# Kernel tuning notes

Hardware: AMD Instinct MI355X
Metric: run time of the kernel (lower is better)

## Reference

```python
import jax, jax.numpy as jnp
import numpy as np

B, NP, DL, DA, H, NB = 8, 81920, 16, 4, 128, 3
DT_TOTAL = DL + DA  # 20
NSTEPS = 4
DT = 0.1


def setup_inputs() -> dict:
    key = jax.random.key(0)
    k1, k2, k3, k4 = jax.random.split(key, 4)
    inputs = jax.random.normal(k1, (B, NP, DT_TOTAL), dtype=jnp.float32)
    neighbours = jax.random.randint(k2, (NP, NB), 0, NP, dtype=jnp.int64)
    fan_in = NB * DT_TOTAL  # 60
    W1 = jax.random.normal(k3, (fan_in, H), dtype=jnp.float32) / np.sqrt(fan_in)
    b1 = jnp.zeros((H,), dtype=jnp.float32)
    W2 = jax.random.normal(k4, (H, DL), dtype=jnp.float32) / np.sqrt(H)
    b2 = jnp.zeros((DL,), dtype=jnp.float32)
    return {"inputs": inputs, "neighbours": neighbours, "W1": W1, "b1": b1, "W2": W2, "b2": b2}


def reference(inputs, neighbours, W1, b1, W2, b2):
    """nsteps of forward Euler: Y[..., :DL] += dt * Phi(gather(Y, neighbours))."""
    Y = inputs
    for _ in range(NSTEPS):
        # neighbour gather: (B, NP, NB, DT_TOTAL)
        Z = Y[:, neighbours, :]
        # shared interaction MLP on flattened neighbourhood features
        Zf = Z.reshape(B, NP, NB * DT_TOTAL)
        h = jnp.tanh(jnp.einsum('bpf,fh->bph', Zf, W1) + b1)
        fZ = jnp.einsum('bph,hd->bpd', h, W2) + b2  # (B, NP, DL)
        # pad with zeros over ancillary dims == update only latent slice
        Y = Y.at[..., :DL].add(DT * fZ)
    return Y
```

## Files before the change

### kernel.cpp

```cpp
#include <hip/hip_runtime.h>

#define B_DIM   8
#define NPTS    81920
#define DTOT    20
#define DT_STEP 0.1f

#define BLOCK 64
#define GRID  5120
#define ITERS 8
#define NFRAG 21
#define FIMG_BYTES 32768
#define TANH_SCALE 2.885390082f

#define MDL_ROW 32
#define MDA_ROW 8

typedef __attribute__((ext_vector_type(8))) short    short8;
typedef __attribute__((ext_vector_type(4))) float    f32x4;
typedef __attribute__((ext_vector_type(2))) unsigned u32x2;
typedef __attribute__((ext_vector_type(4))) unsigned u32x4;
typedef __attribute__((ext_vector_type(2))) short    short2v;

__device__ __forceinline__ unsigned short f2bf(float f) {
    unsigned u = __builtin_bit_cast(unsigned, f);
    u += 0x7FFFu + ((u >> 16) & 1u);
    return (unsigned short)(u >> 16);
}
#if __has_builtin(__builtin_amdgcn_cvt_pk_bf16_f32)
__device__ __forceinline__ unsigned pack2(float a, float b) {
    short2v p = __builtin_amdgcn_cvt_pk_bf16_f32(a, b);
    return __builtin_bit_cast(unsigned, p);
}
#else
__device__ __forceinline__ unsigned pack2(float a, float b) {
    return (unsigned)f2bf(a) | ((unsigned)f2bf(b) << 16);
}
#endif
__device__ __forceinline__ f32x4 unpack4(u32x2 m) {
    f32x4 o;
    o.x = __builtin_bit_cast(float, m.x << 16);
    o.y = __builtin_bit_cast(float, m.x & 0xffff0000u);
    o.z = __builtin_bit_cast(float, m.y << 16);
    o.w = __builtin_bit_cast(float, m.y & 0xffff0000u);
    return o;
}
__device__ __forceinline__ float tanh_folded(float a) {
    float e = __builtin_amdgcn_exp2f(a);
    float r = __builtin_amdgcn_rcpf(1.0f + e);
    return 1.0f - 2.0f * r;
}

__device__ __forceinline__ int feat_of(int ks, int q, int j) {
    if (ks == 0) {
        if (q == 0) return j;
        if (q == 1) return 8 + j;
        if (q == 2) return 20 + j;
        return (j < 4) ? 16 + j : 36 + (j - 4);
    }
    if (q == 0) return 28 + j;
    if (q == 1) return 40 + j;
    if (q == 2) return 48 + j;
    if (j < 4) return 56 + j;
    return (j == 4) ? 60 : 61;
}

__device__ __forceinline__ int hid_of(int ks, int q, int j) {
    return (2 * ks + (j >> 2)) * 16 + q * 4 + (j & 3);
}

__global__ __launch_bounds__(256) void build_mirror(
    const f32x4* __restrict__ in, char* __restrict__ m0dl,
    char* __restrict__ mda, f32x4* __restrict__ outF, int n4,
    const float* __restrict__ W1, const float* __restrict__ b1,
    const float* __restrict__ W2, const float* __restrict__ b2,
    char* __restrict__ img)
{
    const int i = blockIdx.x * 256 + threadIdx.x;
    if (i < n4) {
        f32x4 v = in[i];
        u32x2 o; o.x = pack2(v.x, v.y); o.y = pack2(v.z, v.w);
        const int r = i / 5, c = i % 5;
        if (c < 4) {
            *(u32x2*)(m0dl + (size_t)r * MDL_ROW + c * 8) = o;
        } else {
            *(u32x2*)(mda + (size_t)r * MDA_ROW) = o;
            outF[i] = v;
        }
    }
    if (blockIdx.x == 0) {
        const int t = threadIdx.x, lane = t & 63, g = t >> 6;
        const int l15 = lane & 15, q = lane >> 4;
        for (int f = g; f < NFRAG; f += 4) {
            char* dst = img + (f * 64 + lane) * 16;
            if (f < 16) {
                const int nt = f >> 1, ks = f & 1, m = nt * 16 + l15;
                unsigned short v[8];
                #pragma unroll
                for (int j = 0; j < 8; j++) {
                    const int ft = feat_of(ks, q, j);
                    float x = (ft < 60) ? TANH_SCALE * W1[ft * 128 + m]
                                        : (ft == 60 ? TANH_SCALE * b1[m] : 0.0f);
                    v[j] = f2bf(x);
                }
                *(u32x4*)dst = *(const u32x4*)v;
            } else if (f < 20) {
                const int ks = f - 16;
                unsigned short v[8];
                #pragma unroll
                for (int j = 0; j < 8; j++) {
                    const int H = hid_of(ks, q, j);
                    v[j] = f2bf(DT_STEP * W2[H * 16 + l15]);
                }
                *(u32x4*)dst = *(const u32x4*)v;
            } else {
                f32x4 a = { DT_STEP * b2[q * 4 + 0], DT_STEP * b2[q * 4 + 1],
                            DT_STEP * b2[q * 4 + 2], DT_STEP * b2[q * 4 + 3] };
                *(f32x4*)dst = a;
            }
        }
    }
}

__device__ __forceinline__ void gather3(
    const char* __restrict__ MdlB, const char* __restrict__ MdaB,
    int nx0, int nx1, int nx2,
    int offA, int offB, bool selA, bool selB, bool q3,
    u32x4& A, u32x4& Bv, u32x2& C)
{
    const int rA = selA ? nx1 : nx0;
    const int rB = selB ? nx2 : nx1;
    const char* aA = q3 ? (MdaB + (size_t)nx0 * MDA_ROW)
                        : (MdlB + (size_t)rA * MDL_ROW + offA);
    const char* aB = q3 ? (MdaB + (size_t)nx1 * MDA_ROW)
                        : (MdlB + (size_t)rB * MDL_ROW + offB);
    A  = *(const u32x4*)aA;
    Bv = *(const u32x4*)aB;
    u32x2 c = { 0u, 0u };
    if (q3) c = *(const u32x2*)(MdaB + (size_t)nx2 * MDA_ROW);
    C = c;
}

__global__ __launch_bounds__(BLOCK) void neural_step(
    float* __restrict__ Yout,
    const char* __restrict__ Mdl_in, char* __restrict__ Mdl_out,
    const char* __restrict__ Mda,
    const int* __restrict__ nbr, const char* __restrict__ img,
    const int last)
{
    const int t = threadIdx.x, lane = t & 63;
    const int l15 = lane & 15, q = lane >> 4;
    const bool q3 = (q == 3);
    const bool selA = (q == 2);
    const bool selB = (q == 1) || (q == 2);
    const int offA = (q == 1) ? 16 : 0;
    const int offB = (q == 0) || (q == 2) ? 16 : 0;

    const int bk = blockIdx.x;
    const int bB = bk & 7;
    const int p0 = (bk >> 3) * (ITERS * 16) + l15;
    const size_t rowBase = (size_t)bB * NPTS;
    const char* MdlB = Mdl_in  + (size_t)bB * NPTS * MDL_ROW;
    char*       MdoB = Mdl_out + (size_t)bB * NPTS * MDL_ROW;
    const char* MdaB = Mda     + (size_t)bB * NPTS * MDA_ROW;

    int nx0, nx1, nx2, ny0 = 0, ny1 = 0, ny2 = 0;
    u32x4 gA, gB, nA = {0,0,0,0}, nB = {0,0,0,0};
    u32x2 gC, nC = {0,0};
    u32x2 ownC, ownN = {0u, 0u};
    {
        const int* np = nbr + (size_t)p0 * 3;
        nx0 = np[0]; nx1 = np[1]; nx2 = np[2];
        gather3(MdlB, MdaB, nx0, nx1, nx2, offA, offB, selA, selB, q3,
                gA, gB, gC);
        ownC = *(const u32x2*)(MdlB + (size_t)p0 * MDL_ROW + q * 8);
        const int* np1 = nbr + (size_t)(p0 + 16) * 3;
        nx0 = np1[0]; nx1 = np1[1]; nx2 = np1[2];
    }

    const short8* frg = (const short8*)img;
    short8 B1f[8][2];
    #pragma unroll
    for (int nt = 0; nt < 8; nt++)
        #pragma unroll
        for (int ks = 0; ks < 2; ks++)
            B1f[nt][ks] = frg[(nt * 2 + ks) * 64 + lane];
    short8 W2f[4];
    #pragma unroll
    for (int ks = 0; ks < 4; ks++)
        W2f[ks] = frg[(16 + ks) * 64 + lane];
    const f32x4 acc2init = ((const f32x4*)img)[20 * 64 + lane];

    #pragma unroll
    for (int it = 0; it < ITERS; it++) {
        if (it + 1 < ITERS) {
            ownN = *(const u32x2*)(MdlB + (size_t)(p0 + (it + 1) * 16) * MDL_ROW
                                   + q * 8);
            gather3(MdlB, MdaB, nx0, nx1, nx2, offA, offB, selA, selB, q3,
                    nA, nB, nC);
        }
        if (it + 2 < ITERS) {
            const int* np = nbr + (size_t)(p0 + (it + 2) * 16) * 3;
            ny0 = np[0]; ny1 = np[1]; ny2 = np[2];
        }

        u32x4 u0 = { gA.x, gA.y, q3 ? gB.x : gA.z, q3 ? gB.y : gA.w };
        u32x4 u1 = { q3 ? gC.x : gB.x, q3 ? gC.y : gB.y,
                     q3 ? 0x00003F80u : gB.z, q3 ? 0u : gB.w };
        short8 zb0 = __builtin_bit_cast(short8, u0);
        short8 zb1 = __builtin_bit_cast(short8, u1);

        unsigned hx[8], hy[8];
        #pragma unroll
        for (int nt = 0; nt < 8; nt++) {
            f32x4 acc = { 0.f, 0.f, 0.f, 0.f };
            acc = __builtin_amdgcn_mfma_f32_16x16x32_bf16(B1f[nt][0], zb0, acc, 0, 0, 0);
            acc = __builtin_amdgcn_mfma_f32_16x16x32_bf16(B1f[nt][1], zb1, acc, 0, 0, 0);
            hx[nt] = pack2(tanh_folded(acc[0]), tanh_folded(acc[1]));
            hy[nt] = pack2(tanh_folded(acc[2]), tanh_folded(acc[3]));
        }

        f32x4 acc2 = acc2init;
        #pragma unroll
        for (int ks = 0; ks < 4; ks++) {
            u32x4 hu = { hx[2 * ks], hy[2 * ks], hx[2 * ks + 1], hy[2 * ks + 1] };
            acc2 = __builtin_amdgcn_mfma_f32_16x16x32_bf16(
                W2f[ks], __builtin_bit_cast(short8, hu), acc2, 0, 0, 0);
        }

        f32x4 o = unpack4(ownC);
        o.x += acc2[0]; o.y += acc2[1]; o.z += acc2[2]; o.w += acc2[3];
        if (!last) {
            char* mrow = MdoB + (size_t)(p0 + it * 16) * MDL_ROW;
            u32x2 mw; mw.x = pack2(o.x, o.y); mw.y = pack2(o.z, o.w);
            *(u32x2*)(mrow + q * 8) = mw;
        } else {
            const size_t row = rowBase + (size_t)(p0 + it * 16);
            __builtin_nontemporal_store(o, (f32x4*)(Yout + row * DTOT) + q);
        }

        ownC = ownN;
        gA = nA; gB = nB; gC = nC;
        nx0 = ny0; nx1 = ny1; nx2 = ny2;
    }
}

extern "C" void kernel_launch(void* const* d_in, const int* in_sizes, int n_in,
                              void* d_out, int out_size, void* d_ws, size_t ws_size,
                              hipStream_t stream) {
    const float* inputs = (const float*)d_in[0];
    const int*   nbr    = (const int*)  d_in[1];
    const float* W1     = (const float*)d_in[2];
    const float* b1     = (const float*)d_in[3];
    const float* W2     = (const float*)d_in[4];
    const float* b2     = (const float*)d_in[5];
    float* out = (float*)d_out;

    const size_t MDL_BYTES = (size_t)B_DIM * NPTS * MDL_ROW;
    const size_t MDA_BYTES = (size_t)B_DIM * NPTS * MDA_ROW;
    char* M0 = (char*)d_ws;
    char* M1 = (char*)d_ws + MDL_BYTES;
    char* DA = (char*)d_ws + 2 * MDL_BYTES;
    char* FI = DA + MDA_BYTES;

    const int n4 = B_DIM * NPTS * DTOT / 4;
    build_mirror<<<n4 / 256, 256, 0, stream>>>(
        (const f32x4*)inputs, M0, DA, (f32x4*)out, n4,
        W1, b1, W2, b2, FI);

    const dim3 grid(GRID), block(BLOCK);
    neural_step<<<grid, block, 0, stream>>>(out, M0, M1, DA, nbr, FI, 0);
    neural_step<<<grid, block, 0, stream>>>(out, M1, M0, DA, nbr, FI, 0);
    neural_step<<<grid, block, 0, stream>>>(out, M0, M1, DA, nbr, FI, 0);
    neural_step<<<grid, block, 0, stream>>>(out, M1, M0, DA, nbr, FI, 1);
}
```

Before: 265.4 us.

## Stage MLP weight fragments in LDS with 4-wave blocks

Moves the W1/W2 bf16 MFMA fragments out of per-thread registers into a shared LDS buffer loaded once per 256-thread block. Each block now holds four waves that share the weights, and each wave handles 4 iterations of 16 points instead of 8. This cuts VGPR pressure and the per-wave global weight loads, which could allow higher occupancy. The cost is LDS reads inside the inner MFMA loop, a block-wide barrier, and a shorter software pipeline per wave.

```diff
diff --git a/kernel.cpp b/kernel.cpp
--- a/kernel.cpp
+++ b/kernel.cpp
@@ -5,11 +5,12 @@
 #define DTOT    20
 #define DT_STEP 0.1f
 
-#define BLOCK 64
-#define GRID  5120
-#define ITERS 8
+#define BLOCK 256
+#define GRID  2560
+#define ITERS 4
 #define NFRAG 21
 #define FIMG_BYTES 32768
+#define LDS_W_BYTES 20480
 #define TANH_SCALE 2.885390082f
 
 #define MDL_ROW 32
@@ -147,7 +148,8 @@
     const int* __restrict__ nbr, const char* __restrict__ img,
     const int last)
 {
-    const int t = threadIdx.x, lane = t & 63;
+    __shared__ __align__(16) char sW[LDS_W_BYTES];
+    const int t = threadIdx.x, lane = t & 63, w = t >> 6;
     const int l15 = lane & 15, q = lane >> 4;
     const bool q3 = (q == 3);
     const bool selA = (q == 2);
@@ -157,7 +159,7 @@
 
     const int bk = blockIdx.x;
     const int bB = bk & 7;
-    const int p0 = (bk >> 3) * (ITERS * 16) + l15;
+    const int p0 = (bk >> 3) * (ITERS * 64) + w * 16 + l15;
     const size_t rowBase = (size_t)bB * NPTS;
     const char* MdlB = Mdl_in  + (size_t)bB * NPTS * MDL_ROW;
     char*       MdoB = Mdl_out + (size_t)bB * NPTS * MDL_ROW;
@@ -173,33 +175,32 @@
         gather3(MdlB, MdaB, nx0, nx1, nx2, offA, offB, selA, selB, q3,
                 gA, gB, gC);
         ownC = *(const u32x2*)(MdlB + (size_t)p0 * MDL_ROW + q * 8);
-        const int* np1 = nbr + (size_t)(p0 + 16) * 3;
+        const int* np1 = nbr + (size_t)(p0 + 64) * 3;
         nx0 = np1[0]; nx1 = np1[1]; nx2 = np1[2];
     }
 
-    const short8* frg = (const short8*)img;
-    short8 B1f[8][2];
-    #pragma unroll
-    for (int nt = 0; nt < 8; nt++)
+    {
+        const u32x4* src = (const u32x4*)img;
+        u32x4* dst = (u32x4*)sW;
         #pragma unroll
-        for (int ks = 0; ks < 2; ks++)
-            B1f[nt][ks] = frg[(nt * 2 + ks) * 64 + lane];
-    short8 W2f[4];
-    #pragma unroll
-    for (int ks = 0; ks < 4; ks++)
-        W2f[ks] = frg[(16 + ks) * 64 + lane];
+        for (int k = 0; k < 5; k++)
+            dst[t + k * 256] = src[t + k * 256];
+    }
     const f32x4 acc2init = ((const f32x4*)img)[20 * 64 + lane];
+    __syncthreads();
+
+    const char* sWl = sW + lane * 16;
 
     #pragma unroll
     for (int it = 0; it < ITERS; it++) {
         if (it + 1 < ITERS) {
-            ownN = *(const u32x2*)(MdlB + (size_t)(p0 + (it + 1) * 16) * MDL_ROW
+            ownN = *(const u32x2*)(MdlB + (size_t)(p0 + (it + 1) * 64) * MDL_ROW
                                    + q * 8);
             gather3(MdlB, MdaB, nx0, nx1, nx2, offA, offB, selA, selB, q3,
                     nA, nB, nC);
         }
         if (it + 2 < ITERS) {
-            const int* np = nbr + (size_t)(p0 + (it + 2) * 16) * 3;
+            const int* np = nbr + (size_t)(p0 + (it + 2) * 64) * 3;
             ny0 = np[0]; ny1 = np[1]; ny2 = np[2];
         }
 
@@ -212,9 +213,11 @@
         unsigned hx[8], hy[8];
         #pragma unroll
         for (int nt = 0; nt < 8; nt++) {
+            short8 a0 = *(const short8*)(sWl + (nt * 2 + 0) * 1024);
+            short8 a1 = *(const short8*)(sWl + (nt * 2 + 1) * 1024);
             f32x4 acc = { 0.f, 0.f, 0.f, 0.f };
-            acc = __builtin_amdgcn_mfma_f32_16x16x32_bf16(B1f[nt][0], zb0, acc, 0, 0, 0);
-            acc = __builtin_amdgcn_mfma_f32_16x16x32_bf16(B1f[nt][1], zb1, acc, 0, 0, 0);
+            acc = __builtin_amdgcn_mfma_f32_16x16x32_bf16(a0, zb0, acc, 0, 0, 0);
+            acc = __builtin_amdgcn_mfma_f32_16x16x32_bf16(a1, zb1, acc, 0, 0, 0);
             hx[nt] = pack2(tanh_folded(acc[0]), tanh_folded(acc[1]));
             hy[nt] = pack2(tanh_folded(acc[2]), tanh_folded(acc[3]));
         }
@@ -222,19 +225,20 @@
         f32x4 acc2 = acc2init;
         #pragma unroll
         for (int ks = 0; ks < 4; ks++) {
+            short8 wf = *(const short8*)(sWl + 16384 + ks * 1024);
             u32x4 hu = { hx[2 * ks], hy[2 * ks], hx[2 * ks + 1], hy[2 * ks + 1] };
             acc2 = __builtin_amdgcn_mfma_f32_16x16x32_bf16(
-                W2f[ks], __builtin_bit_cast(short8, hu), acc2, 0, 0, 0);
+                wf, __builtin_bit_cast(short8, hu), acc2, 0, 0, 0);
         }
 
         f32x4 o = unpack4(ownC);
         o.x += acc2[0]; o.y += acc2[1]; o.z += acc2[2]; o.w += acc2[3];
         if (!last) {
-            char* mrow = MdoB + (size_t)(p0 + it * 16) * MDL_ROW;
+            char* mrow = MdoB + (size_t)(p0 + it * 64) * MDL_ROW;
             u32x2 mw; mw.x = pack2(o.x, o.y); mw.y = pack2(o.z, o.w);
             *(u32x2*)(mrow + q * 8) = mw;
         } else {
-            const size_t row = rowBase + (size_t)(p0 + it * 16);
+            const size_t row = rowBase + (size_t)(p0 + it * 64);
             __builtin_nontemporal_store(o, (f32x4*)(Yout + row * DTOT) + q);
         }
 
```

Measured after the change: 249.7 us. 1.06x faster.
